# Kernel optimization log

Hardware: AMD Instinct MI355X
Metric: run time of the kernel (lower is better)

The kernel has to match this reference:

```python
import jax, jax.numpy as jnp
import numpy as np

K = 9           # kernel_size * dilation (dilation=1 -> stride-1 slice is identity)
BN_EPS = 1e-5   # fresh BatchNorm2d (eval): running_mean=0, running_var=1
L2_EPS = 1e-12  # torch F.normalize eps


def setup_inputs() -> dict:
    key = jax.random.key(0)
    k1, k2 = jax.random.split(key, 2)
    B, C, H, W = 4, 192, 56, 56
    Cout = 384
    x = jax.random.normal(k1, (B, C, H, W), jnp.float32)
    conv_w = jax.random.normal(k2, (Cout, 2 * C), jnp.float32) * 0.05  # 1x1 conv weight
    conv_b = jnp.zeros((Cout,), jnp.float32)
    bn_gamma = jnp.ones((Cout,), jnp.float32)
    bn_beta = jnp.zeros((Cout,), jnp.float32)
    return dict(x=x, conv_w=conv_w, conv_b=conv_b, bn_gamma=bn_gamma, bn_beta=bn_beta)


def _knn_idx(xf, k):
    """xf: (B,C,N). L2-normalize channels, pairwise sq-dist, top-k nearest. -> (B,N,k) int32."""
    xn = xf / jnp.maximum(jnp.linalg.norm(xf, axis=1, keepdims=True), L2_EPS)
    pts = xn.transpose(0, 2, 1)                       # (B,N,C)
    sq = jnp.sum(pts * pts, axis=-1)                  # (B,N)
    dist = sq[:, :, None] - 2.0 * jnp.einsum('bnc,bmc->bnm', pts, pts) + sq[:, None, :]
    _, idx = jax.lax.top_k(-dist, k)                  # smallest distance first
    return idx


def reference(x, conv_w, conv_b, bn_gamma, bn_beta):
    B, C, H, W = x.shape
    N = H * W
    xf = x.reshape(B, C, N)                           # (B,C,N,1) squeezed
    nn_idx = _knn_idx(jax.lax.stop_gradient(xf), K)   # KNN built under no_grad

    xt = xf.transpose(0, 2, 1)                        # (B,N,C)
    x_j = jax.vmap(lambda f, i: f[i])(xt, nn_idx)     # (B,N,K,C) neighbor gather
    x_i = jnp.broadcast_to(xt[:, :, None, :], (B, N, K, C))
    feat = jnp.concatenate([x_i, x_j - x_i], axis=-1)  # (B,N,K,2C) edge features

    # BasicConv: 1x1 conv + BatchNorm2d (eval, mean=0,var=1) + GELU
    z = jnp.einsum('bnkc,oc->bnko', feat, conv_w) + conv_b
    z = z * (bn_gamma / np.sqrt(1.0 + BN_EPS)) + bn_beta
    z = jax.nn.gelu(z, approximate=False)

    out = jnp.max(z, axis=2)                          # max over K neighbors -> (B,N,O)
    out = out.transpose(0, 2, 1).reshape(B, -1, H, W)

    center = jnp.broadcast_to(jnp.arange(N, dtype=nn_idx.dtype)[None, :, None], (B, N, K))
    edge_index = jnp.stack([nn_idx, center], axis=0)  # (2,B,N,K), debug=True output
    return out, edge_index
```

## Files before the change

### kernel.cpp

```cpp
#include <hip/hip_runtime.h>
#include <hip/hip_bf16.h>
#include <math.h>

#define B_    4
#define C_    192
#define NPT   3136
#define CO_   384
#define KNN   9
#define K2    16
#define NROWS (B_*NPT)
#define SD    10

typedef _Float16 half8 __attribute__((ext_vector_type(8)));
typedef float    f32x4 __attribute__((ext_vector_type(4)));

__device__ __forceinline__ float u2f(unsigned short u) {
    unsigned int t = ((unsigned int)u) << 16;
    float f; __builtin_memcpy(&f, &t, 4); return f;
}
__device__ __forceinline__ unsigned short f2u(float f) {
    __hip_bfloat16 h = __float2bfloat16(f);
    unsigned short u; __builtin_memcpy(&u, &h, 2); return u;
}
__device__ __forceinline__ float gelu_exact(float y) {
    return 0.5f * y * (1.0f + erff(y * 0.70710678118654752f));
}
__device__ __forceinline__ unsigned long long dkey(double d) {
    long long sb = __double_as_longlong(d);
    unsigned long long u = (unsigned long long)sb;
    return (sb < 0) ? ~u : (u | 0x8000000000000000ULL);
}

__global__ __launch_bounds__(256) void k_norm(
    const float* __restrict__ x,
    float* __restrict__ invn32, double* __restrict__ invn64,
    double* __restrict__ sqd, float* __restrict__ nrm32)
{
    __shared__ double part[4][64];
    int wave = threadIdx.x >> 6, lane = threadIdx.x & 63;
    int p0 = blockIdx.x * 64;
    int row = p0 + lane;
    int b = row / NPT, n = row % NPT;
    const float* xb = x + (size_t)b * C_ * NPT + n;
    double S = 0.0;
    int c0 = wave * 48;
    for (int c = c0; c < c0 + 48; ++c) {
        double v = (double)xb[(size_t)c * NPT];
        S = fma(v, v, S);
    }
    part[wave][lane] = S;
    __syncthreads();
    if (threadIdx.x < 64) {
        double T = ((part[0][lane] + part[1][lane]) + part[2][lane])
                 + part[3][lane];
        double nrm = sqrt(T);
        if (nrm < 1e-12) nrm = 1e-12;
        double iv = 1.0 / nrm;
        int prow = p0 + lane;
        invn64[prow] = iv;
        invn32[prow] = (float)iv;
        sqd[prow] = iv * iv * T;
        nrm32[prow] = (float)nrm;
    }
}

__global__ __launch_bounds__(256) void k_xpose(
    const float* __restrict__ x, float* __restrict__ xT,
    const float* __restrict__ invn32, _Float16* __restrict__ packed)
{
    __shared__ float t[32][33];
    int blk = blockIdx.x;
    int b  = blk / 588;
    int r  = blk % 588;
    int ct = r / 98, nt = r % 98;
    int c0 = ct * 32, n0 = nt * 32;
    int tid = threadIdx.x;
    int tx = tid & 31, ty8 = tid >> 5;
    const float* xb = x + (size_t)b * C_ * NPT;
#pragma unroll
    for (int e = 0; e < 4; ++e) {
        int cc = ty8 + e * 8;
        t[cc][tx] = xb[(size_t)(c0 + cc) * NPT + n0 + tx];
    }
    __syncthreads();
#pragma unroll
    for (int e = 0; e < 4; ++e) {
        int nn = ty8 + e * 8;
        xT[(size_t)(b * NPT + n0 + nn) * C_ + c0 + tx] = t[tx][nn];
    }
    if (tid < 128) {
        int f = tid >> 6, l = tid & 63;
        int pt = f * 16 + (l & 15);
        float iv = invn32[(size_t)b * NPT + n0 + pt];
        int cb = (l >> 4) * 8;
        half8 h;
#pragma unroll
        for (int e = 0; e < 8; ++e)
            h[e] = (_Float16)(t[cb + e][pt] * iv);
        size_t idx = ((((size_t)(b * 196 + nt * 2 + f)) * 6 + ct) * 64 + l) * 8;
        *(half8*)(packed + idx) = h;
    }
}

__global__ __launch_bounds__(256) void k_wpack(
    const float* __restrict__ cw, _Float16* __restrict__ wpk)
{
    int t = blockIdx.x * 256 + threadIdx.x;
    if (t >= 48 * 6 * 64) return;
    int l  = t & 63;
    int tk = t >> 6;
    int kk = tk % 6, ot = tk / 6;
    int hsel = ot / 24;
    int o = (ot % 24) * 16 + (l & 15);
    int k = kk * 32 + (l >> 4) * 8;
    half8 h;
#pragma unroll
    for (int e = 0; e < 8; ++e) {
        float w2 = cw[(size_t)o * 384 + C_ + k + e];
        float wv = hsel ? w2 : (cw[(size_t)o * 384 + k + e] - w2);
        h[e] = (_Float16)wv;
    }
    *(half8*)(wpk + (size_t)t * 8) = h;
}

__global__ __launch_bounds__(256) void k_screen_mfma(
    const _Float16* __restrict__ packed, unsigned* __restrict__ cand)
{
    __shared__ unsigned md[64][8 * SD + 1];
    int blk   = blockIdx.x;
    int chunk = blk / 196;
    int t2    = blk % 196;
    int b     = t2 / 49;
    int itile = t2 % 49;
    int tid   = threadIdx.x;
    int wave  = tid >> 6, lane = tid & 63;
    int it    = itile * 4 + wave;

    const _Float16* pb = packed + ((size_t)(b * 196 + it) * 6) * 512 + lane * 8;
    half8 bf[6];
#pragma unroll
    for (int kk = 0; kk < 6; ++kk)
        bf[kk] = *(const half8*)(pb + kk * 512);

    int jt0 = chunk * 28;
    const int ntj = 28;

    unsigned bdA[SD], bdB[SD];
#pragma unroll
    for (int q = 0; q < SD; ++q) { bdA[q] = 0u; bdB[q] = 0u; }

    const _Float16* pa_base =
        packed + ((size_t)(b * 196 + jt0) * 6) * 512 + lane * 8;

    half8 af[6];
#pragma unroll
    for (int kk = 0; kk < 6; ++kk)
        af[kk] = *(const half8*)(pa_base + kk * 512);

    for (int jt = 0; jt < ntj; ++jt) {
        f32x4 acc = {0.f, 0.f, 0.f, 0.f};
#pragma unroll
        for (int kk = 0; kk < 6; ++kk)
            acc = __builtin_amdgcn_mfma_f32_16x16x32_f16(af[kk], bf[kk], acc, 0, 0, 0);

        if (jt + 1 < ntj) {
            const _Float16* pn = pa_base + (size_t)(jt + 1) * 6 * 512;
#pragma unroll
            for (int kk = 0; kk < 6; ++kk)
                af[kk] = *(const half8*)(pn + kk * 512);
        }

        unsigned jb = (unsigned)((jt0 + jt) * 16 + (lane >> 4) * 4);
#pragma unroll
        for (int q = 0; q < 2; ++q) {
            unsigned fb = __float_as_uint(acc[q] + 2.0f);
            unsigned c = (fb & 0xFFFFF000u) | (jb + (unsigned)q);
#pragma unroll
            for (int t = 0; t < SD; ++t) {
                unsigned old = bdA[t];
                unsigned mx = old > c ? old : c;
                c           = old > c ? c : old;
                bdA[t] = mx;
            }
        }
#pragma unroll
        for (int q = 2; q < 4; ++q) {
            unsigned fb = __float_as_uint(acc[q] + 2.0f);
            unsigned c = (fb & 0xFFFFF000u) | (jb + (unsigned)q);
#pragma unroll
            for (int t = 0; t < SD; ++t) {
                unsigned old = bdB[t];
                unsigned mx = old > c ? old : c;
                c           = old > c ? c : old;
                bdB[t] = mx;
            }
        }
    }

    int ir = wave * 16 + (lane & 15);
    int g  = lane >> 4;
#pragma unroll
    for (int q = 0; q < SD; ++q) {
        md[ir][(g * 2 + 0) * SD + q] = bdA[q];
        md[ir][(g * 2 + 1) * SD + q] = bdB[q];
    }
    __syncthreads();

    if (tid < 64) {
        int h[8] = {0, 0, 0, 0, 0, 0, 0, 0};
        size_t rowi = (size_t)b * NPT + itile * 64 + tid;
        unsigned* cp = cand + rowi * 64 + chunk * 9;
        const unsigned* rd = &md[tid][0];
        for (int s = 0; s < 9; ++s) {
            unsigned best = 0u; int bg = 0;
#pragma unroll
            for (int g2 = 0; g2 < 8; ++g2) {
                unsigned v = (h[g2] < SD) ? rd[g2 * SD + h[g2]] : 0u;
                if (v > best) { best = v; bg = g2; }
            }
            cp[s] = best;
            h[bg]++;
        }
        if (chunk == 0)
            cand[rowi * 64 + 63] = 0u;
    }
}

__global__ __launch_bounds__(256) void k_refine(
    const float* __restrict__ xT, const double* __restrict__ invn64,
    const double* __restrict__ sqd, const unsigned* __restrict__ cand32,
    float* __restrict__ e0)
{
    __shared__ unsigned km[4][64];
    __shared__ int    icand[4][K2];
    __shared__ double civ[4][K2];
    __shared__ double csq[4][K2];
    __shared__ unsigned long long kbuf[4][K2];
    __shared__ float  xi[4][C_];
    int wave = threadIdx.x >> 6;
    int lane = threadIdx.x & 63;
    int row  = blockIdx.x * 4 + wave;
    int b    = row / NPT;
    size_t bN = (size_t)b * NPT;

    unsigned kc = cand32[(size_t)row * 64 + lane];
    km[wave][lane] = kc;
    const float* xiRow = xT + (size_t)row * C_;
    xi[wave][lane]       = xiRow[lane];
    xi[wave][lane + 64]  = xiRow[lane + 64];
    xi[wave][lane + 128] = xiRow[lane + 128];
    __syncthreads();

    int keyrank = 0;
#pragma unroll
    for (int m = 0; m < 64; ++m)
        keyrank += (km[wave][m] > kc) ? 1 : 0;
    if (keyrank < K2)
        icand[wave][keyrank] = (int)(kc & 0xFFFu);
    __syncthreads();
    if (lane < K2) {
        int j = icand[wave][lane];
        civ[wave][lane] = invn64[bN + j];
        csq[wave][lane] = sqd[bN + j];
    }
    __syncthreads();

    int sub = lane & 7, cg = lane >> 3;
    double ivi = invn64[row], sqi = sqd[row];
    const float* xw = &xi[wave][sub * 4];

    float4 h0a, h0b, h0c;
    {
        int j0 = icand[wave][cg];
        const float* p = xT + (bN + j0) * C_ + sub * 4;
        h0a = *(const float4*)&p[0];
        h0b = *(const float4*)&p[32];
        h0c = *(const float4*)&p[64];
    }

#pragma unroll
    for (int cc = 0; cc < K2 / 8; ++cc) {
        int cidx = cc * 8 + cg;
        int jcur = icand[wave][cidx];
        const float* pc = xT + (bN + jcur) * C_ + sub * 4;
        float4 h1a = *(const float4*)&pc[96];
        float4 h1b = *(const float4*)&pc[128];
        float4 h1c = *(const float4*)&pc[160];

        double d0 = 0.0, d1 = 0.0, d2 = 0.0, d3 = 0.0;
        {
            float4 xq;
            xq = *(const float4*)&xw[0];
            d0 = fma((double)xq.x, (double)h0a.x, d0);
            d1 = fma((double)xq.y, (double)h0a.y, d1);
            d2 = fma((double)xq.z, (double)h0a.z, d2);
            d3 = fma((double)xq.w, (double)h0a.w, d3);
            xq = *(const float4*)&xw[32];
            d0 = fma((double)xq.x, (double)h0b.x, d0);
            d1 = fma((double)xq.y, (double)h0b.y, d1);
            d2 = fma((double)xq.z, (double)h0b.z, d2);
            d3 = fma((double)xq.w, (double)h0b.w, d3);
            xq = *(const float4*)&xw[64];
            d0 = fma((double)xq.x, (double)h0c.x, d0);
            d1 = fma((double)xq.y, (double)h0c.y, d1);
            d2 = fma((double)xq.z, (double)h0c.z, d2);
            d3 = fma((double)xq.w, (double)h0c.w, d3);
        }
        if (cc < K2 / 8 - 1) {
            int jn = icand[wave][cidx + 8];
            const float* pn = xT + (bN + jn) * C_ + sub * 4;
            h0a = *(const float4*)&pn[0];
            h0b = *(const float4*)&pn[32];
            h0c = *(const float4*)&pn[64];
        }
        {
            float4 xq;
            xq = *(const float4*)&xw[96];
            d0 = fma((double)xq.x, (double)h1a.x, d0);
            d1 = fma((double)xq.y, (double)h1a.y, d1);
            d2 = fma((double)xq.z, (double)h1a.z, d2);
            d3 = fma((double)xq.w, (double)h1a.w, d3);
            xq = *(const float4*)&xw[128];
            d0 = fma((double)xq.x, (double)h1b.x, d0);
            d1 = fma((double)xq.y, (double)h1b.y, d1);
            d2 = fma((double)xq.z, (double)h1b.z, d2);
            d3 = fma((double)xq.w, (double)h1b.w, d3);
            xq = *(const float4*)&xw[160];
            d0 = fma((double)xq.x, (double)h1c.x, d0);
            d1 = fma((double)xq.y, (double)h1c.y, d1);
            d2 = fma((double)xq.z, (double)h1c.z, d2);
            d3 = fma((double)xq.w, (double)h1c.w, d3);
        }
        double dot = (d0 + d1) + (d2 + d3);
        dot += __shfl_xor(dot, 1);
        dot += __shfl_xor(dot, 2);
        dot += __shfl_xor(dot, 4);
        if (sub == 0) {
            double dist = sqi + csq[wave][cidx]
                        - 2.0 * (ivi * civ[wave][cidx] * dot);
            kbuf[wave][cidx] = dkey(dist);
        }
    }
    __syncthreads();

    if (lane < K2) {
        unsigned long long kd = kbuf[wave][lane];
        int jme = icand[wave][lane];
        int rank = 0;
#pragma unroll
        for (int m = 0; m < K2; ++m) {
            unsigned long long km2 = kbuf[wave][m];
            int jm = icand[wave][m];
            rank += ((km2 < kd) || (km2 == kd && jm < jme)) ? 1 : 0;
        }
        if (rank < KNN)
            e0[(size_t)row * KNN + rank] = (float)jme;
    }
}

__global__ __launch_bounds__(256) void k_gemm_mfma(
    const _Float16* __restrict__ packed, const _Float16* __restrict__ wpk,
    const float* __restrict__ nrm32, const float* __restrict__ cb,
    unsigned short* __restrict__ Bh, float* __restrict__ Zf)
{
    int pt   = blockIdx.x;
    int wave = threadIdx.x >> 6, lane = threadIdx.x & 63;
    int hsel = wave >> 1;
    int og   = wave & 1;

    const _Float16* px = packed + (size_t)pt * 6 * 512 + lane * 8;
    half8 pf[6];
#pragma unroll
    for (int kk = 0; kk < 6; ++kk) pf[kk] = *(const half8*)(px + kk * 512);

    float s = nrm32[pt * 16 + (lane & 15)];
    size_t row0 = (size_t)pt * 16 + (lane & 15);
    int olane = (lane >> 4) * 4;

    int ot0 = hsel * 24 + og * 12;
    const _Float16* wb = wpk + (size_t)ot0 * 6 * 512 + lane * 8;

    half8 wf[6];
#pragma unroll
    for (int kk = 0; kk < 6; ++kk) wf[kk] = *(const half8*)(wb + kk * 512);

    for (int t = 0; t < 12; ++t) {
        f32x4 acc = {0.f, 0.f, 0.f, 0.f};
#pragma unroll
        for (int kk = 0; kk < 6; ++kk)
            acc = __builtin_amdgcn_mfma_f32_16x16x32_f16(wf[kk], pf[kk], acc, 0, 0, 0);

        if (t < 11) {
            const _Float16* wn = wb + (size_t)(t + 1) * 6 * 512;
#pragma unroll
            for (int kk = 0; kk < 6; ++kk)
                wf[kk] = *(const half8*)(wn + kk * 512);
        }

        int o = (og * 12 + t) * 16 + olane;
        if (hsel == 0) {
            float4 cbv = *(const float4*)&cb[o];
            float4 zv;
            zv.x = acc[0] * s + cbv.x; zv.y = acc[1] * s + cbv.y;
            zv.z = acc[2] * s + cbv.z; zv.w = acc[3] * s + cbv.w;
            *(float4*)&Zf[row0 * 384 + o] = zv;
        } else {
            ushort4 pk;
            pk.x = f2u(acc[0] * s); pk.y = f2u(acc[1] * s);
            pk.z = f2u(acc[2] * s); pk.w = f2u(acc[3] * s);
            *(ushort4*)&Bh[row0 * 384 + o] = pk;
        }
    }
}

__global__ __launch_bounds__(256) void k_out2(
    const float* __restrict__ e0, const float* __restrict__ gam,
    const float* __restrict__ bet, float* __restrict__ out,
    const unsigned short* __restrict__ Bh, const float* __restrict__ Zf,
    float* __restrict__ e1)
{
    __shared__ int jidx[64 * KNN];
    int blk = blockIdx.x;
    int b   = blk / 294;
    int r   = blk % 294;
    int nt  = r % 49, ot = r / 49;
    int n0 = nt * 64, o0 = ot * 64;
    int tid = threadIdx.x;
    int tx = tid & 15, ty = tid >> 4;

    for (int e = tid; e < 64 * KNN; e += 256)
        jidx[e] = (int)e0[((size_t)b * NPT + n0 + e / KNN) * KNN + e % KNN];

    {
        int p = blk * 96 + tid;
        if (tid < 96) e1[p] = (float)((p / KNN) % NPT);
    }

    const float inv_s = 0.9999950000374997f;
    float gs[4], bts[4];
#pragma unroll
    for (int v = 0; v < 4; ++v) {
        int o = o0 + tx * 4 + v;
        gs[v]  = gam[o] * inv_s;
        bts[v] = bet[o];
    }
    __syncthreads();

    float best[4][4];
#pragma unroll
    for (int u = 0; u < 4; ++u) {
        float4 z = *(const float4*)
            &Zf[(size_t)(b * NPT + n0 + ty * 4 + u) * 384 + o0 + tx * 4];
        float zA[4] = {z.x, z.y, z.z, z.w};

        float ymin[4], ymax[4];
#pragma unroll
        for (int v = 0; v < 4; ++v) { ymin[v] = 1e30f; ymax[v] = -1e30f; }

        const int* jr = &jidx[(ty * 4 + u) * KNN];
#pragma unroll
        for (int k = 0; k < KNN; ++k) {
            int j = jr[k];
            ushort4 g = *(const ushort4*)
                &Bh[(size_t)(b * NPT + j) * 384 + o0 + tx * 4];
            float bvv[4] = {u2f(g.x), u2f(g.y), u2f(g.z), u2f(g.w)};
#pragma unroll
            for (int v = 0; v < 4; ++v) {
                float y = fmaf(zA[v] + bvv[v], gs[v], bts[v]);
                ymin[v] = fminf(ymin[v], y);
                ymax[v] = fmaxf(ymax[v], y);
            }
        }
#pragma unroll
        for (int v = 0; v < 4; ++v)
            best[u][v] = fmaxf(gelu_exact(ymin[v]), gelu_exact(ymax[v]));
    }

#pragma unroll
    for (int v = 0; v < 4; ++v) {
        int o = o0 + tx * 4 + v;
        float4 pk = {best[0][v], best[1][v], best[2][v], best[3][v]};
        *(float4*)(out + ((size_t)(b * CO_ + o)) * NPT + n0 + ty * 4) = pk;
    }
}

__global__ __launch_bounds__(256) void k_gemmB(
    const float* __restrict__ x, const float* __restrict__ cw,
    void* __restrict__ Bq, int bbase, int bcol0, int ldB, int storeBf16,
    int botiles, int bstrideBytes)
{
    int per = 49 * botiles;
    int blk = blockIdx.x;
    int bi  = blk / per;
    int r   = blk % per;
    int b   = bbase + bi;
    int bm = r % 49;
    int bo = r / 49;
    int m0 = bm * 64;
    char* Bp = (char*)Bq + (size_t)bi * (size_t)bstrideBytes;

    __shared__ float Xt[16][68];
    __shared__ float Wt[16][68];
    int tid = threadIdx.x;
    int tx = tid & 15, ty = tid >> 4;
    const float* xb = x + (size_t)b * C_ * NPT;
    float acc[4][4];
#pragma unroll
    for (int u = 0; u < 4; ++u)
#pragma unroll
        for (int v = 0; v < 4; ++v) acc[u][v] = 0.f;

    for (int ct = 0; ct < 12; ++ct) {
        int c0 = ct * 16;
        {
            int cc = tid >> 4, n4 = (tid & 15) * 4;
            *(float4*)&Xt[cc][n4] =
                *(const float4*)&xb[(size_t)(c0 + cc) * NPT + m0 + n4];
        }
        {
            int oo = tid >> 2, c4 = (tid & 3) * 4;
            int o = bcol0 + bo * 64 + oo;
            float4 w = *(const float4*)&cw[(size_t)o * 384 + C_ + c0 + c4];
            Wt[c4 + 0][oo] = w.x; Wt[c4 + 1][oo] = w.y;
            Wt[c4 + 2][oo] = w.z; Wt[c4 + 3][oo] = w.w;
        }
        __syncthreads();
#pragma unroll
        for (int cc = 0; cc < 16; ++cc) {
            float4 av = *(const float4*)&Xt[cc][ty * 4];
            float4 bv = *(const float4*)&Wt[cc][tx * 4];
            float a_[4] = {av.x, av.y, av.z, av.w};
            float b_[4] = {bv.x, bv.y, bv.z, bv.w};
#pragma unroll
            for (int u = 0; u < 4; ++u)
#pragma unroll
                for (int v = 0; v < 4; ++v)
                    acc[u][v] = fmaf(a_[u], b_[v], acc[u][v]);
        }
        __syncthreads();
    }
    if (!storeBf16) {
        float* Bf = (float*)Bp;
#pragma unroll
        for (int u = 0; u < 4; ++u) {
            float4 pk = {acc[u][0], acc[u][1], acc[u][2], acc[u][3]};
            *(float4*)&Bf[(size_t)(m0 + ty * 4 + u) * ldB + bo * 64 + tx * 4] = pk;
        }
    } else {
        unsigned short* Bh = (unsigned short*)Bp;
#pragma unroll
        for (int u = 0; u < 4; ++u) {
            ushort4 pk;
            pk.x = f2u(acc[u][0]); pk.y = f2u(acc[u][1]);
            pk.z = f2u(acc[u][2]); pk.w = f2u(acc[u][3]);
            *(ushort4*)&Bh[(size_t)(m0 + ty * 4 + u) * ldB + bo * 64 + tx * 4] = pk;
        }
    }
}

__global__ __launch_bounds__(256) void k_outA(
    const float* __restrict__ x, const float* __restrict__ cw,
    const float* __restrict__ e0, const float* __restrict__ cb,
    const float* __restrict__ gam, const float* __restrict__ bet,
    float* __restrict__ out, const void* __restrict__ Bq,
    int bbase, int o0base, int bcol0, int ldB, int readBf16,
    int botiles, int bstrideBytes)
{
    int per = 49 * botiles;
    int blk = blockIdx.x;
    int bi  = blk / per;
    int r   = blk % per;
    int b   = bbase + bi;
    int nt = r % 49, ot = r / 49;
    int n0 = nt * 64, o0 = o0base + ot * 64;
    const char* Bp = (const char*)Bq + (size_t)bi * (size_t)bstrideBytes;

    __shared__ float Xi[16][68];
    __shared__ float Wd[16][68];
    __shared__ int jidx[64 * KNN];
    int tid = threadIdx.x;
    int tx = tid & 15, ty = tid >> 4;
    const float* xb = x + (size_t)b * C_ * NPT;

    for (int e = tid; e < 64 * KNN; e += 256)
        jidx[e] = (int)e0[((size_t)b * NPT + n0 + e / KNN) * KNN + e % KNN];

    float zA[4][4];
#pragma unroll
    for (int u = 0; u < 4; ++u)
#pragma unroll
        for (int v = 0; v < 4; ++v) zA[u][v] = 0.f;

    for (int ct = 0; ct < 12; ++ct) {
        int c0 = ct * 16;
        {
            int cc = tid >> 4, n4 = (tid & 15) * 4;
            *(float4*)&Xi[cc][n4] =
                *(const float4*)&xb[(size_t)(c0 + cc) * NPT + n0 + n4];
        }
        {
            int oo = tid >> 2, c4 = (tid & 3) * 4;
            int o = o0 + oo;
            float4 w1 = *(const float4*)&cw[(size_t)o * 384 + c0 + c4];
            float4 w2 = *(const float4*)&cw[(size_t)o * 384 + C_ + c0 + c4];
            Wd[c4 + 0][oo] = w1.x - w2.x; Wd[c4 + 1][oo] = w1.y - w2.y;
            Wd[c4 + 2][oo] = w1.z - w2.z; Wd[c4 + 3][oo] = w1.w - w2.w;
        }
        __syncthreads();
#pragma unroll
        for (int cc = 0; cc < 16; ++cc) {
            float4 av = *(const float4*)&Xi[cc][ty * 4];
            float4 bv = *(const float4*)&Wd[cc][tx * 4];
            float a_[4] = {av.x, av.y, av.z, av.w};
            float b_[4] = {bv.x, bv.y, bv.z, bv.w};
#pragma unroll
            for (int u = 0; u < 4; ++u)
#pragma unroll
                for (int v = 0; v < 4; ++v)
                    zA[u][v] = fmaf(a_[u], b_[v], zA[u][v]);
        }
        __syncthreads();
    }

    const float inv_s = 0.9999950000374997f;
    float gs[4], bts[4], cbs[4];
#pragma unroll
    for (int v = 0; v < 4; ++v) {
        int o = o0 + tx * 4 + v;
        gs[v]  = gam[o] * inv_s;
        bts[v] = bet[o];
        cbs[v] = cb[o];
    }

    float best[4][4];
#pragma unroll
    for (int u = 0; u < 4; ++u)
#pragma unroll
        for (int v = 0; v < 4; ++v) best[u][v] = -1e30f;

    int obB = o0 - bcol0;
    for (int k = 0; k < KNN; ++k) {
#pragma unroll
        for (int u = 0; u < 4; ++u) {
            int j = jidx[(ty * 4 + u) * KNN + k];
            float bvv[4];
            if (!readBf16) {
                float4 g = *(const float4*)
                    ((const float*)Bp + (size_t)j * ldB + obB + tx * 4);
                bvv[0] = g.x; bvv[1] = g.y; bvv[2] = g.z; bvv[3] = g.w;
            } else {
                ushort4 g = *(const ushort4*)
                    ((const unsigned short*)Bp + (size_t)j * ldB + obB + tx * 4);
                bvv[0] = u2f(g.x); bvv[1] = u2f(g.y);
                bvv[2] = u2f(g.z); bvv[3] = u2f(g.w);
            }
#pragma unroll
            for (int v = 0; v < 4; ++v) {
                float z = zA[u][v] + bvv[v] + cbs[v];
                float y = fmaf(z, gs[v], bts[v]);
                float ge = 0.5f * y * (1.0f + erff(y * 0.70710678118654752f));
                best[u][v] = fmaxf(best[u][v], ge);
            }
        }
    }

#pragma unroll
    for (int v = 0; v < 4; ++v) {
        int o = o0 + tx * 4 + v;
        float4 pk = {best[0][v], best[1][v], best[2][v], best[3][v]};
        *(float4*)(out + ((size_t)(b * CO_ + o)) * NPT + n0 + ty * 4) = pk;
    }
}

__global__ __launch_bounds__(256) void k_center(float* __restrict__ e1)
{
    int p = blockIdx.x * 256 + threadIdx.x;
    if (p >= NROWS * KNN) return;
    e1[p] = (float)((p / KNN) % NPT);
}

extern "C" void kernel_launch(void* const* d_in, const int* in_sizes, int n_in,
                              void* d_out, int out_size, void* d_ws, size_t ws_size,
                              hipStream_t stream)
{
    const float* x   = (const float*)d_in[0];
    const float* cw  = (const float*)d_in[1];
    const float* cb  = (const float*)d_in[2];
    const float* gam = (const float*)d_in[3];
    const float* bet = (const float*)d_in[4];

    float* ou   = (float*)d_out;
    float* out0 = ou;
    double* invn64 = (double*)d_out;
    double* sqd    = (double*)((char*)d_out + 100352);
    float*  invn32 = (float*)((char*)d_out + 200704);
    unsigned* cand32 = (unsigned*)((char*)d_out + 250880);
    _Float16* packed = (_Float16*)((char*)d_out + 3462144);
    float*    nrm32  = (float*)((char*)d_out + 8279040);
    _Float16* wpk    = (_Float16*)((char*)d_out + 8329216);
    float* xT = ou + 2408448;
    float* e0 = ou + 4816896;
    float* e1 = ou + 4929792;

    k_norm       <<<NROWS / 64, 256, 0, stream>>>(x, invn32, invn64, sqd, nrm32);
    k_xpose      <<<B_ * 6 * 98, 256, 0, stream>>>(x, xT, invn32, packed);
    k_screen_mfma<<<7 * B_ * 49, 256, 0, stream>>>(packed, cand32);
    k_refine     <<<NROWS / 4, 256, 0, stream>>>(xT, invn64, sqd, cand32, e0);

    const size_t BH_BYTES = (size_t)NROWS * 384 * 2;
    const size_t ZF_BYTES = (size_t)NROWS * 384 * 4;
    const int    BSTRIDE  = NPT * CO_ * 4;

    if (ws_size >= BH_BYTES + ZF_BYTES) {
        unsigned short* wsB = (unsigned short*)d_ws;
        float* wsZ = (float*)((char*)d_ws + BH_BYTES);
        k_wpack    <<<72, 256, 0, stream>>>(cw, wpk);
        k_gemm_mfma<<<784, 256, 0, stream>>>(packed, wpk, nrm32, cb, wsB, wsZ);
        k_out2     <<<B_ * 49 * 6, 256, 0, stream>>>(e0, gam, bet, out0,
                                                     wsB, wsZ, e1);
    } else if (ws_size >= ZF_BYTES) {
        k_gemmB<<<B_ * 49 * 6, 256, 0, stream>>>(
            x, cw, d_ws, 0, 0, 384, 0, 6, BSTRIDE);
        k_outA <<<B_ * 49 * 6, 256, 0, stream>>>(
            x, cw, e0, cb, gam, bet, out0, (const void*)d_ws,
            0, 0, 0, 384, 0, 6, BSTRIDE);
        k_center<<<(NROWS * KNN + 255) / 256, 256, 0, stream>>>(e1);
    } else {
        k_gemmB<<<2 * 49 * 6, 256, 0, stream>>>(
            x, cw, (void*)ou, 2, 0, 384, 0, 6, BSTRIDE);
        k_outA <<<2 * 49 * 6, 256, 0, stream>>>(
            x, cw, e0, cb, gam, bet, out0, (const void*)ou,
            2, 0, 0, 384, 0, 6, BSTRIDE);
        k_gemmB<<<49 * 6, 256, 0, stream>>>(
            x, cw, (void*)ou, 1, 0, 384, 0, 6, 0);
        k_outA <<<49 * 6, 256, 0, stream>>>(
            x, cw, e0, cb, gam, bet, out0, (const void*)ou,
            1, 0, 0, 384, 0, 6, 0);
        k_gemmB<<<49 * 3, 256, 0, stream>>>(
            x, cw, (void*)ou, 0, 192, 192, 1, 3, 0);
        k_outA <<<49 * 3, 256, 0, stream>>>(
            x, cw, e0, cb, gam, bet, out0, (const void*)ou,
            0, 192, 192, 192, 1, 3, 0);
        k_gemmB<<<49 * 2, 256, 0, stream>>>(
            x, cw, (void*)ou, 0, 64, 128, 1, 2, 0);
        k_outA <<<49 * 2, 256, 0, stream>>>(
            x, cw, e0, cb, gam, bet, out0, (const void*)ou,
            0, 64, 64, 128, 1, 2, 0);
        k_gemmB<<<49 * 1, 256, 0, stream>>>(
            x, cw, (void*)e1, 0, 0, 64, 1, 1, 0);
        k_outA <<<49 * 1, 256, 0, stream>>>(
            x, cw, e0, cb, gam, bet, out0, (const void*)e1,
            0, 0, 0, 64, 1, 1, 0);
        k_center<<<(NROWS * KNN + 255) / 256, 256, 0, stream>>>(e1);
    }
}
```

Baseline: 185.0 us.

## Merge KNN screening and edge-feature GEMM into one heterogeneous launch

The KNN screening kernel and the independent MFMA GEMM are combined into one grid, with block index selecting the role, and the weight packing moves ahead of the transpose. The two phases can then overlap on the GPU and one launch boundary, with its tail idle time, goes away. In exchange the GEMM blocks now reserve the screening shared-memory array, which can reduce occupancy, and refine now waits for the merged kernel.

```diff
diff --git a/kernel.cpp b/kernel.cpp
--- a/kernel.cpp
+++ b/kernel.cpp
@@ -10,6 +10,7 @@
 #define K2    16
 #define NROWS (B_*NPT)
 #define SD    10
+#define NSCRB (7*196)
 
 typedef _Float16 half8 __attribute__((ext_vector_type(8)));
 typedef float    f32x4 __attribute__((ext_vector_type(4)));
@@ -123,11 +124,11 @@
     *(half8*)(wpk + (size_t)t * 8) = h;
 }
 
-__global__ __launch_bounds__(256) void k_screen_mfma(
-    const _Float16* __restrict__ packed, unsigned* __restrict__ cand)
-{
-    __shared__ unsigned md[64][8 * SD + 1];
-    int blk   = blockIdx.x;
+__device__ __forceinline__ void dev_screen(
+    unsigned (*md)[8 * SD + 1],
+    const _Float16* __restrict__ packed, unsigned* __restrict__ cand,
+    int blk)
+{
     int chunk = blk / 196;
     int t2    = blk % 196;
     int b     = t2 / 49;
@@ -224,6 +225,88 @@
         if (chunk == 0)
             cand[rowi * 64 + 63] = 0u;
     }
+}
+
+__device__ __forceinline__ void dev_gemm(
+    const _Float16* __restrict__ packed, const _Float16* __restrict__ wpk,
+    const float* __restrict__ nrm32, const float* __restrict__ cb,
+    unsigned short* __restrict__ Bh, float* __restrict__ Zf, int pt)
+{
+    int wave = threadIdx.x >> 6, lane = threadIdx.x & 63;
+    int hsel = wave >> 1;
+    int og   = wave & 1;
+
+    const _Float16* px = packed + (size_t)pt * 6 * 512 + lane * 8;
+    half8 pf[6];
+#pragma unroll
+    for (int kk = 0; kk < 6; ++kk) pf[kk] = *(const half8*)(px + kk * 512);
+
+    float s = nrm32[pt * 16 + (lane & 15)];
+    size_t row0 = (size_t)pt * 16 + (lane & 15);
+    int olane = (lane >> 4) * 4;
+
+    int ot0 = hsel * 24 + og * 12;
+    const _Float16* wb = wpk + (size_t)ot0 * 6 * 512 + lane * 8;
+
+    half8 wf[6];
+#pragma unroll
+    for (int kk = 0; kk < 6; ++kk) wf[kk] = *(const half8*)(wb + kk * 512);
+
+    for (int t = 0; t < 12; ++t) {
+        f32x4 acc = {0.f, 0.f, 0.f, 0.f};
+#pragma unroll
+        for (int kk = 0; kk < 6; ++kk)
+            acc = __builtin_amdgcn_mfma_f32_16x16x32_f16(wf[kk], pf[kk], acc, 0, 0, 0);
+
+        if (t < 11) {
+            const _Float16* wn = wb + (size_t)(t + 1) * 6 * 512;
+#pragma unroll
+            for (int kk = 0; kk < 6; ++kk)
+                wf[kk] = *(const half8*)(wn + kk * 512);
+        }
+
+        int o = (og * 12 + t) * 16 + olane;
+        if (hsel == 0) {
+            float4 cbv = *(const float4*)&cb[o];
+            float4 zv;
+            zv.x = acc[0] * s + cbv.x; zv.y = acc[1] * s + cbv.y;
+            zv.z = acc[2] * s + cbv.z; zv.w = acc[3] * s + cbv.w;
+            *(float4*)&Zf[row0 * 384 + o] = zv;
+        } else {
+            ushort4 pk;
+            pk.x = f2u(acc[0] * s); pk.y = f2u(acc[1] * s);
+            pk.z = f2u(acc[2] * s); pk.w = f2u(acc[3] * s);
+            *(ushort4*)&Bh[row0 * 384 + o] = pk;
+        }
+    }
+}
+
+__global__ __launch_bounds__(256) void k_screen_mfma(
+    const _Float16* __restrict__ packed, unsigned* __restrict__ cand)
+{
+    __shared__ unsigned md[64][8 * SD + 1];
+    dev_screen(md, packed, cand, blockIdx.x);
+}
+
+__global__ __launch_bounds__(256) void k_screen_gemm(
+    const _Float16* __restrict__ packed, unsigned* __restrict__ cand,
+    const _Float16* __restrict__ wpk, const float* __restrict__ nrm32,
+    const float* __restrict__ cb,
+    unsigned short* __restrict__ Bh, float* __restrict__ Zf)
+{
+    __shared__ unsigned md[64][8 * SD + 1];
+    if (blockIdx.x < NSCRB)
+        dev_screen(md, packed, cand, blockIdx.x);
+    else
+        dev_gemm(packed, wpk, nrm32, cb, Bh, Zf, blockIdx.x - NSCRB);
+}
+
+__global__ __launch_bounds__(256) void k_gemm_mfma(
+    const _Float16* __restrict__ packed, const _Float16* __restrict__ wpk,
+    const float* __restrict__ nrm32, const float* __restrict__ cb,
+    unsigned short* __restrict__ Bh, float* __restrict__ Zf)
+{
+    dev_gemm(packed, wpk, nrm32, cb, Bh, Zf, blockIdx.x);
 }
 
 __global__ __launch_bounds__(256) void k_refine(
@@ -358,61 +441,6 @@
     }
 }
 
-__global__ __launch_bounds__(256) void k_gemm_mfma(
-    const _Float16* __restrict__ packed, const _Float16* __restrict__ wpk,
-    const float* __restrict__ nrm32, const float* __restrict__ cb,
-    unsigned short* __restrict__ Bh, float* __restrict__ Zf)
-{
-    int pt   = blockIdx.x;
-    int wave = threadIdx.x >> 6, lane = threadIdx.x & 63;
-    int hsel = wave >> 1;
-    int og   = wave & 1;
-
-    const _Float16* px = packed + (size_t)pt * 6 * 512 + lane * 8;
-    half8 pf[6];
-#pragma unroll
-    for (int kk = 0; kk < 6; ++kk) pf[kk] = *(const half8*)(px + kk * 512);
-
-    float s = nrm32[pt * 16 + (lane & 15)];
-    size_t row0 = (size_t)pt * 16 + (lane & 15);
-    int olane = (lane >> 4) * 4;
-
-    int ot0 = hsel * 24 + og * 12;
-    const _Float16* wb = wpk + (size_t)ot0 * 6 * 512 + lane * 8;
-
-    half8 wf[6];
-#pragma unroll
-    for (int kk = 0; kk < 6; ++kk) wf[kk] = *(const half8*)(wb + kk * 512);
-
-    for (int t = 0; t < 12; ++t) {
-        f32x4 acc = {0.f, 0.f, 0.f, 0.f};
-#pragma unroll
-        for (int kk = 0; kk < 6; ++kk)
-            acc = __builtin_amdgcn_mfma_f32_16x16x32_f16(wf[kk], pf[kk], acc, 0, 0, 0);
-
-        if (t < 11) {
-            const _Float16* wn = wb + (size_t)(t + 1) * 6 * 512;
-#pragma unroll
-            for (int kk = 0; kk < 6; ++kk)
-                wf[kk] = *(const half8*)(wn + kk * 512);
-        }
-
-        int o = (og * 12 + t) * 16 + olane;
-        if (hsel == 0) {
-            float4 cbv = *(const float4*)&cb[o];
-            float4 zv;
-            zv.x = acc[0] * s + cbv.x; zv.y = acc[1] * s + cbv.y;
-            zv.z = acc[2] * s + cbv.z; zv.w = acc[3] * s + cbv.w;
-            *(float4*)&Zf[row0 * 384 + o] = zv;
-        } else {
-            ushort4 pk;
-            pk.x = f2u(acc[0] * s); pk.y = f2u(acc[1] * s);
-            pk.z = f2u(acc[2] * s); pk.w = f2u(acc[3] * s);
-            *(ushort4*)&Bh[row0 * 384 + o] = pk;
-        }
-    }
-}
-
 __global__ __launch_bounds__(256) void k_out2(
     const float* __restrict__ e0, const float* __restrict__ gam,
     const float* __restrict__ bet, float* __restrict__ out,
@@ -702,23 +730,27 @@
     float* e0 = ou + 4816896;
     float* e1 = ou + 4929792;
 
-    k_norm       <<<NROWS / 64, 256, 0, stream>>>(x, invn32, invn64, sqd, nrm32);
-    k_xpose      <<<B_ * 6 * 98, 256, 0, stream>>>(x, xT, invn32, packed);
-    k_screen_mfma<<<7 * B_ * 49, 256, 0, stream>>>(packed, cand32);
-    k_refine     <<<NROWS / 4, 256, 0, stream>>>(xT, invn64, sqd, cand32, e0);
-
     const size_t BH_BYTES = (size_t)NROWS * 384 * 2;
     const size_t ZF_BYTES = (size_t)NROWS * 384 * 4;
     const int    BSTRIDE  = NPT * CO_ * 4;
-
-    if (ws_size >= BH_BYTES + ZF_BYTES) {
+    int fastpath = ws_size >= BH_BYTES + ZF_BYTES;
+
+    k_norm <<<NROWS / 64, 256, 0, stream>>>(x, invn32, invn64, sqd, nrm32);
+    if (fastpath)
+        k_wpack<<<72, 256, 0, stream>>>(cw, wpk);
+    k_xpose<<<B_ * 6 * 98, 256, 0, stream>>>(x, xT, invn32, packed);
+
+    if (fastpath) {
         unsigned short* wsB = (unsigned short*)d_ws;
         float* wsZ = (float*)((char*)d_ws + BH_BYTES);
-        k_wpack    <<<72, 256, 0, stream>>>(cw, wpk);
-        k_gemm_mfma<<<784, 256, 0, stream>>>(packed, wpk, nrm32, cb, wsB, wsZ);
-        k_out2     <<<B_ * 49 * 6, 256, 0, stream>>>(e0, gam, bet, out0,
-                                                     wsB, wsZ, e1);
+        k_screen_gemm<<<NSCRB + 784, 256, 0, stream>>>(
+            packed, cand32, wpk, nrm32, cb, wsB, wsZ);
+        k_refine<<<NROWS / 4, 256, 0, stream>>>(xT, invn64, sqd, cand32, e0);
+        k_out2  <<<B_ * 49 * 6, 256, 0, stream>>>(e0, gam, bet, out0,
+                                                  wsB, wsZ, e1);
     } else if (ws_size >= ZF_BYTES) {
+        k_screen_mfma<<<NSCRB, 256, 0, stream>>>(packed, cand32);
+        k_refine<<<NROWS / 4, 256, 0, stream>>>(xT, invn64, sqd, cand32, e0);
         k_gemmB<<<B_ * 49 * 6, 256, 0, stream>>>(
             x, cw, d_ws, 0, 0, 384, 0, 6, BSTRIDE);
         k_outA <<<B_ * 49 * 6, 256, 0, stream>>>(
@@ -726,6 +758,8 @@
             0, 0, 0, 384, 0, 6, BSTRIDE);
         k_center<<<(NROWS * KNN + 255) / 256, 256, 0, stream>>>(e1);
     } else {
+        k_screen_mfma<<<NSCRB, 256, 0, stream>>>(packed, cand32);
+        k_refine<<<NROWS / 4, 256, 0, stream>>>(xT, invn64, sqd, cand32, e0);
         k_gemmB<<<2 * 49 * 6, 256, 0, stream>>>(
             x, cw, (void*)ou, 2, 0, 384, 0, 6, BSTRIDE);
         k_outA <<<2 * 49 * 6, 256, 0, stream>>>(
```

Result: faster. 174.2 us (-5.8%).
